# Kernel optimization log

Measured on AMD Instinct MI355X. Metric: run time of the kernel, lower is better.

## Reference

```python
import jax, jax.numpy as jnp
import numpy as np
from jax import lax

STATE = 16
DNA = 4


def _sobel_kernels():
    sx = jnp.array([[-1.0, 0.0, 1.0], [-2.0, 0.0, 2.0], [-1.0, 0.0, 1.0]], dtype=jnp.float32)
    sy = sx.T
    # depthwise kernels, OIHW with I=1, O=STATE
    kx = jnp.tile(sx[None, None], (STATE, 1, 1, 1))
    ky = jnp.tile(sy[None, None], (STATE, 1, 1, 1))
    return kx, ky


def _depthwise(x, k):
    # x: [B, C, H, W], k: [C, 1, 3, 3]; torch conv2d == cross-correlation == lax conv
    return lax.conv_general_dilated(
        x, k, window_strides=(1, 1), padding='SAME',
        feature_group_count=STATE,
        dimension_numbers=('NCHW', 'OIHW', 'NCHW'))


def setup_inputs() -> dict:
    key = jax.random.key(0)
    k1, k2, k3, k4 = jax.random.split(key, 4)
    B, H, W = 16, 256, 256
    x = jax.random.normal(k1, (B, STATE, H, W), dtype=jnp.float32)
    dna = jax.random.normal(k2, (B, DNA, H, W), dtype=jnp.float32)
    fan1 = STATE * 3 + DNA  # 52
    w1 = jax.random.normal(k3, (128, fan1), dtype=jnp.float32) * (1.0 / np.sqrt(fan1))
    w2 = jax.random.normal(k4, (STATE, 128), dtype=jnp.float32) * (1.0 / np.sqrt(128.0))
    return {"x": x, "dna": dna, "w1": w1, "w2": w2}


def reference(x, dna, w1, w2):
    kx, ky = _sobel_kernels()
    grad_x = _depthwise(x, kx)
    grad_y = _depthwise(x, ky)
    feat = jnp.concatenate([x, grad_x, grad_y, dna], axis=1)  # [B, 52, H, W]
    h = jnp.einsum('oc,bchw->bohw', w1, feat)  # 1x1 conv, bias=False
    h = jax.nn.relu(h)
    update = jnp.einsum('oc,bchw->bohw', w2, h)  # 1x1 conv to state_size
    return update
```

## Files before the change

### kernel.cpp

```cpp
#include <hip/hip_runtime.h>
#include <hip/hip_bf16.h>

#define STATE 16
#define DNA_C 4
#define HID   128
#define FAN1  52
#define HH    256
#define WW    256
#define HW    (HH * WW)

typedef unsigned short u16;
typedef unsigned int   u32;
typedef short bf8 __attribute__((ext_vector_type(8)));
typedef float f32x4 __attribute__((ext_vector_type(4)));

typedef __attribute__((address_space(1))) const void gv_t;
typedef __attribute__((address_space(3))) void lv_t;

__device__ __forceinline__ u32 pk(float a, float b) {
    __hip_bfloat162 t = __float22bfloat162_rn(make_float2(a, b));
    union { __hip_bfloat162 h; u32 u; } c; c.h = t; return c.u;
}
__device__ __forceinline__ u16 f2bf(float f) {
    union { __hip_bfloat16 h; u16 u; } c; c.h = __float2bfloat16(f); return c.u;
}

__global__ void prep_weights(const float* __restrict__ w1, const float* __restrict__ w2,
                             u16* __restrict__ wb) {
    int i = blockIdx.x * 256 + threadIdx.x;
    if (i < 128 * 64) {
        int p = i >> 6, knew = i & 63;
        int m = p >> 4, g = (p >> 2) & 3, r = p & 3;
        int hrow = 32 * (m >> 1) + 8 * g + 4 * (m & 1) + r;
        int w = knew >> 4, t = knew & 15;
        float v = 0.f;
        if (t < 4)        v = w1[hrow * FAN1 + 4 * w + t];
        else if (t < 8)   v = w1[hrow * FAN1 + 16 + 4 * w + (t - 4)];
        else if (t < 12)  v = w1[hrow * FAN1 + 32 + 4 * w + (t - 8)];
        else if (t == 12) v = w1[hrow * FAN1 + 48 + w];
        wb[i] = f2bf(v);
    } else if (i < 128 * 64 + 16 * 128) {
        wb[i] = f2bf(w2[i - 128 * 64]);
    }
}

__global__ __launch_bounds__(256, 2) void update_net24(
    const float* __restrict__ x,
    const float* __restrict__ dna,
    const u16*   __restrict__ wb,
    float* __restrict__ out,
    int nrows)
{
    __shared__ __align__(16) float raw_lds[3][STATE * WW];
    __shared__ __align__(16) u16 feat_lds[256 * 64];

    const int tid  = threadIdx.x;
    const int lane = tid & 63;
    const int wv   = tid >> 6;
    const int fj   = lane & 15;
    const int fg   = lane >> 4;
    const int f4   = fj >> 2;
    const int px0  = lane * 4;

    const u16* w1b = wb;
    const u16* w2b = wb + 128 * 64;
    bf8 a1[8][2];
    #pragma unroll
    for (int m = 0; m < 8; ++m) {
        #pragma unroll
        for (int kt = 0; kt < 2; ++kt)
            a1[m][kt] = *(const bf8*)&w1b[(16 * m + fj) * 64 + 32 * kt + 8 * fg];
    }
    bf8 a2[4];
    #pragma unroll
    for (int kt = 0; kt < 4; ++kt)
        a2[kt] = *(const bf8*)&w2b[fj * 128 + 32 * kt + 8 * fg];

    const f32x4 z0 = {0.f, 0.f, 0.f, 0.f};

    const int q  = nrows / gridDim.x;
    const int start = blockIdx.x * q;
    const int b  = start >> 8;
    const int y0 = start & 255;

    auto stage_row = [&](int yy, int slot) {
        const float* g = x + (((size_t)(b * STATE + 4 * wv)) * HH + yy) * WW + px0;
        float* l = &raw_lds[slot][(4 * wv) * WW];
        #pragma unroll
        for (int c = 0; c < 4; ++c)
            __builtin_amdgcn_global_load_lds((gv_t*)(g + (size_t)c * HW),
                                             (lv_t*)(l + c * WW), 16, 0, 0);
    };

    if (y0 > 0) stage_row(y0 - 1, (y0 - 1) % 3);
    stage_row(y0, y0 % 3);
    stage_row(y0 + 1, (y0 + 1) % 3);
    asm volatile("s_waitcnt vmcnt(0)" ::: "memory");
    __builtin_amdgcn_sched_barrier(0);

    for (int it = 0; it < q; ++it) {
        const int y = y0 + it;
        const bool ht = (y > 0), hb = (y < HH - 1);
        const int sm = y % 3, st3 = (y + 2) % 3, sb = (y + 1) % 3;

        {
            const f32x4 dnv = *(const f32x4*)(dna + (((size_t)(b * DNA_C + wv)) * HH + y) * WW + px0);
            const float* rm_ = &raw_lds[sm][(4 * wv) * WW + px0];
            const float* rt_ = &raw_lds[st3][(4 * wv) * WW + px0];
            const float* rb_ = &raw_lds[sb][(4 * wv) * WW + px0];

            f32x4 xm[4], gx[4], gy[4];
            #pragma unroll
            for (int c = 0; c < 4; ++c) {
                f32x4 m4 = *(const f32x4*)(rm_ + c * WW);
                f32x4 t4 = {0.f,0.f,0.f,0.f}, b4 = {0.f,0.f,0.f,0.f};
                if (ht) t4 = *(const f32x4*)(rt_ + c * WW);
                if (hb) b4 = *(const f32x4*)(rb_ + c * WW);
                f32x4 cs, d;
                #pragma unroll
                for (int i = 0; i < 4; ++i) {
                    cs[i] = fmaf(2.f, m4[i], t4[i] + b4[i]);
                    d[i]  = b4[i] - t4[i];
                }
                float csL = __shfl_up(cs[3], 1);
                float csR = __shfl_down(cs[0], 1);
                float dL  = __shfl_up(d[3], 1);
                float dR  = __shfl_down(d[0], 1);
                if (lane == 0)  { csL = 0.f; dL = 0.f; }
                if (lane == 63) { csR = 0.f; dR = 0.f; }
                xm[c] = m4;
                gx[c][0] = cs[1] - csL;   gx[c][1] = cs[2] - cs[0];
                gx[c][2] = cs[3] - cs[1]; gx[c][3] = csR - cs[2];
                gy[c][0] = fmaf(2.f, d[0], dL + d[1]);
                gy[c][1] = fmaf(2.f, d[1], d[0] + d[2]);
                gy[c][2] = fmaf(2.f, d[2], d[1] + d[3]);
                gy[c][3] = fmaf(2.f, d[3], d[2] + dR);
            }

            const int s = lane & 7;
            #pragma unroll
            for (int i = 0; i < 4; ++i) {
                u16* rowp = &feat_lds[(px0 + i) * 64];
                uint4 c0 = make_uint4(pk(xm[0][i], xm[1][i]), pk(xm[2][i], xm[3][i]),
                                      pk(gx[0][i], gx[1][i]), pk(gx[2][i], gx[3][i]));
                uint4 c1 = make_uint4(pk(gy[0][i], gy[1][i]), pk(gy[2][i], gy[3][i]),
                                      pk(dnv[i], 0.f), 0u);
                *(uint4*)&rowp[8 * ((2 * wv)     ^ s)] = c0;
                *(uint4*)&rowp[8 * ((2 * wv + 1) ^ s)] = c1;
            }
        }

        __syncthreads();

        if (it + 1 < q && y + 2 <= HH - 1)
            stage_row(y + 2, (y + 2) % 3);

        #pragma unroll
        for (int g4 = 0; g4 < 4; ++g4) {
            const int r  = wv * 64 + g4 * 16 + fj;
            const int sg = (4 * g4 + f4) & 7;
            bf8 b0 = *(const bf8*)&feat_lds[r * 64 + 8 * ((0 + fg) ^ sg)];
            bf8 b1 = *(const bf8*)&feat_lds[r * 64 + 8 * ((4 + fg) ^ sg)];

            u32 w[8][2];
            #pragma unroll
            for (int mh = 0; mh < 2; ++mh) {
                f32x4 hc[4];
                #pragma unroll
                for (int mm = 0; mm < 4; ++mm) {
                    const int m = mh * 4 + mm;
                    f32x4 z = __builtin_amdgcn_mfma_f32_16x16x32_bf16(a1[m][0], b0, z0, 0, 0, 0);
                    hc[mm] = __builtin_amdgcn_mfma_f32_16x16x32_bf16(a1[m][1], b1, z, 0, 0, 0);
                }
                #pragma unroll
                for (int mm = 0; mm < 4; ++mm) {
                    const int m = mh * 4 + mm;
                    w[m][0] = pk(fmaxf(hc[mm][0], 0.f), fmaxf(hc[mm][1], 0.f));
                    w[m][1] = pk(fmaxf(hc[mm][2], 0.f), fmaxf(hc[mm][3], 0.f));
                }
            }

            f32x4 uacc;
            #pragma unroll
            for (int kt = 0; kt < 4; ++kt) {
                union { u32 u[4]; bf8 v; } bb;
                bb.u[0] = w[2 * kt][0];
                bb.u[1] = w[2 * kt][1];
                bb.u[2] = w[2 * kt + 1][0];
                bb.u[3] = w[2 * kt + 1][1];
                uacc = __builtin_amdgcn_mfma_f32_16x16x32_bf16(a2[kt], bb.v,
                                                               (kt == 0) ? z0 : uacc, 0, 0, 0);
            }

            const int xo = wv * 64 + g4 * 16 + fj;
            float* po = out + (((size_t)(b * STATE + 4 * fg)) * HH + y) * WW + xo;
            #pragma unroll
            for (int rr2 = 0; rr2 < 4; ++rr2)
                po[(size_t)rr2 * HW] = uacc[rr2];
        }

        __syncthreads();
    }
}

extern "C" void kernel_launch(void* const* d_in, const int* in_sizes, int n_in,
                              void* d_out, int out_size, void* d_ws, size_t ws_size,
                              hipStream_t stream) {
    const float* x   = (const float*)d_in[0];
    const float* dna = (const float*)d_in[1];
    const float* w1  = (const float*)d_in[2];
    const float* w2  = (const float*)d_in[3];
    float* out = (float*)d_out;
    u16* wb = (u16*)d_ws;

    prep_weights<<<dim3(40), dim3(256), 0, stream>>>(w1, w2, wb);

    const int B = in_sizes[0] / (STATE * HH * WW);
    const int nrows = B * HH;
    const int grid = 512;
    update_net24<<<dim3(grid), dim3(256), 0, stream>>>(x, dna, wb, out, nrows);
}
```

Baseline: 52.85 us.

## Double block size to 8 waves, each handling 2 channels and 32 pixels

```diff
diff --git a/kernel.cpp b/kernel.cpp
--- a/kernel.cpp
+++ b/kernel.cpp
@@ -32,19 +32,19 @@
         int p = i >> 6, knew = i & 63;
         int m = p >> 4, g = (p >> 2) & 3, r = p & 3;
         int hrow = 32 * (m >> 1) + 8 * g + 4 * (m & 1) + r;
-        int w = knew >> 4, t = knew & 15;
+        int w = knew >> 3, s = knew & 7;
         float v = 0.f;
-        if (t < 4)        v = w1[hrow * FAN1 + 4 * w + t];
-        else if (t < 8)   v = w1[hrow * FAN1 + 16 + 4 * w + (t - 4)];
-        else if (t < 12)  v = w1[hrow * FAN1 + 32 + 4 * w + (t - 8)];
-        else if (t == 12) v = w1[hrow * FAN1 + 48 + w];
+        if (s < 2)                 v = w1[hrow * FAN1 + 2 * w + s];
+        else if (s < 4)            v = w1[hrow * FAN1 + 16 + 2 * w + (s - 2)];
+        else if (s < 6)            v = w1[hrow * FAN1 + 32 + 2 * w + (s - 4)];
+        else if (s == 6 && w < 4)  v = w1[hrow * FAN1 + 48 + w];
         wb[i] = f2bf(v);
     } else if (i < 128 * 64 + 16 * 128) {
         wb[i] = f2bf(w2[i - 128 * 64]);
     }
 }
 
-__global__ __launch_bounds__(256, 2) void update_net24(
+__global__ __launch_bounds__(512, 2) void update_net26(
     const float* __restrict__ x,
     const float* __restrict__ dna,
     const u16*   __restrict__ wb,
@@ -59,8 +59,8 @@
     const int wv   = tid >> 6;
     const int fj   = lane & 15;
     const int fg   = lane >> 4;
-    const int f4   = fj >> 2;
     const int px0  = lane * 4;
+    const int sw   = lane & 7;
 
     const u16* w1b = wb;
     const u16* w2b = wb + 128 * 64;
@@ -84,10 +84,10 @@
     const int y0 = start & 255;
 
     auto stage_row = [&](int yy, int slot) {
-        const float* g = x + (((size_t)(b * STATE + 4 * wv)) * HH + yy) * WW + px0;
-        float* l = &raw_lds[slot][(4 * wv) * WW];
+        const float* g = x + (((size_t)(b * STATE + 2 * wv)) * HH + yy) * WW + px0;
+        float* l = &raw_lds[slot][(2 * wv) * WW];
         #pragma unroll
-        for (int c = 0; c < 4; ++c)
+        for (int c = 0; c < 2; ++c)
             __builtin_amdgcn_global_load_lds((gv_t*)(g + (size_t)c * HW),
                                              (lv_t*)(l + c * WW), 16, 0, 0);
     };
@@ -97,6 +97,7 @@
     stage_row(y0 + 1, (y0 + 1) % 3);
     asm volatile("s_waitcnt vmcnt(0)" ::: "memory");
     __builtin_amdgcn_sched_barrier(0);
+    __syncthreads();
 
     for (int it = 0; it < q; ++it) {
         const int y = y0 + it;
@@ -104,14 +105,16 @@
         const int sm = y % 3, st3 = (y + 2) % 3, sb = (y + 1) % 3;
 
         {
-            const f32x4 dnv = *(const f32x4*)(dna + (((size_t)(b * DNA_C + wv)) * HH + y) * WW + px0);
-            const float* rm_ = &raw_lds[sm][(4 * wv) * WW + px0];
-            const float* rt_ = &raw_lds[st3][(4 * wv) * WW + px0];
-            const float* rb_ = &raw_lds[sb][(4 * wv) * WW + px0];
-
-            f32x4 xm[4], gx[4], gy[4];
-            #pragma unroll
-            for (int c = 0; c < 4; ++c) {
+            f32x4 dnv = {0.f, 0.f, 0.f, 0.f};
+            if (wv < DNA_C)
+                dnv = *(const f32x4*)(dna + (((size_t)(b * DNA_C + wv)) * HH + y) * WW + px0);
+            const float* rm_ = &raw_lds[sm][(2 * wv) * WW + px0];
+            const float* rt_ = &raw_lds[st3][(2 * wv) * WW + px0];
+            const float* rb_ = &raw_lds[sb][(2 * wv) * WW + px0];
+
+            f32x4 xm[2], gx[2], gy[2];
+            #pragma unroll
+            for (int c = 0; c < 2; ++c) {
                 f32x4 m4 = *(const f32x4*)(rm_ + c * WW);
                 f32x4 t4 = {0.f,0.f,0.f,0.f}, b4 = {0.f,0.f,0.f,0.f};
                 if (ht) t4 = *(const f32x4*)(rt_ + c * WW);
@@ -137,16 +140,13 @@
                 gy[c][3] = fmaf(2.f, d[3], d[2] + dR);
             }
 
-            const int s = lane & 7;
             #pragma unroll
             for (int i = 0; i < 4; ++i) {
-                u16* rowp = &feat_lds[(px0 + i) * 64];
-                uint4 c0 = make_uint4(pk(xm[0][i], xm[1][i]), pk(xm[2][i], xm[3][i]),
-                                      pk(gx[0][i], gx[1][i]), pk(gx[2][i], gx[3][i]));
-                uint4 c1 = make_uint4(pk(gy[0][i], gy[1][i]), pk(gy[2][i], gy[3][i]),
-                                      pk(dnv[i], 0.f), 0u);
-                *(uint4*)&rowp[8 * ((2 * wv)     ^ s)] = c0;
-                *(uint4*)&rowp[8 * ((2 * wv + 1) ^ s)] = c1;
+                uint4 qv = make_uint4(pk(xm[0][i], xm[1][i]),
+                                      pk(gx[0][i], gx[1][i]),
+                                      pk(gy[0][i], gy[1][i]),
+                                      pk(dnv[i], 0.f));
+                *(uint4*)&feat_lds[(px0 + i) * 64 + 8 * (wv ^ sw)] = qv;
             }
         }
 
@@ -154,15 +154,16 @@
 
         if (it + 1 < q && y + 2 <= HH - 1)
             stage_row(y + 2, (y + 2) % 3);
+        __builtin_amdgcn_sched_barrier(0);
 
         #pragma unroll
-        for (int g4 = 0; g4 < 4; ++g4) {
-            const int r  = wv * 64 + g4 * 16 + fj;
-            const int sg = (4 * g4 + f4) & 7;
-            bf8 b0 = *(const bf8*)&feat_lds[r * 64 + 8 * ((0 + fg) ^ sg)];
+        for (int g2 = 0; g2 < 2; ++g2) {
+            const int r  = 32 * wv + g2 * 16 + fj;
+            const int sg = (r >> 2) & 7;
+            bf8 b0 = *(const bf8*)&feat_lds[r * 64 + 8 * (fg ^ sg)];
             bf8 b1 = *(const bf8*)&feat_lds[r * 64 + 8 * ((4 + fg) ^ sg)];
 
-            u32 w[8][2];
+            f32x4 uacc;
             #pragma unroll
             for (int mh = 0; mh < 2; ++mh) {
                 f32x4 hc[4];
@@ -172,31 +173,29 @@
                     f32x4 z = __builtin_amdgcn_mfma_f32_16x16x32_bf16(a1[m][0], b0, z0, 0, 0, 0);
                     hc[mm] = __builtin_amdgcn_mfma_f32_16x16x32_bf16(a1[m][1], b1, z, 0, 0, 0);
                 }
+                u32 w[4][2];
                 #pragma unroll
                 for (int mm = 0; mm < 4; ++mm) {
-                    const int m = mh * 4 + mm;
-                    w[m][0] = pk(fmaxf(hc[mm][0], 0.f), fmaxf(hc[mm][1], 0.f));
-                    w[m][1] = pk(fmaxf(hc[mm][2], 0.f), fmaxf(hc[mm][3], 0.f));
+                    w[mm][0] = pk(fmaxf(hc[mm][0], 0.f), fmaxf(hc[mm][1], 0.f));
+                    w[mm][1] = pk(fmaxf(hc[mm][2], 0.f), fmaxf(hc[mm][3], 0.f));
+                }
+                #pragma unroll
+                for (int j = 0; j < 2; ++j) {
+                    union { u32 u[4]; bf8 v; } bb;
+                    bb.u[0] = w[2 * j][0];
+                    bb.u[1] = w[2 * j][1];
+                    bb.u[2] = w[2 * j + 1][0];
+                    bb.u[3] = w[2 * j + 1][1];
+                    uacc = __builtin_amdgcn_mfma_f32_16x16x32_bf16(
+                        a2[2 * mh + j], bb.v, (mh == 0 && j == 0) ? z0 : uacc, 0, 0, 0);
                 }
             }
 
-            f32x4 uacc;
-            #pragma unroll
-            for (int kt = 0; kt < 4; ++kt) {
-                union { u32 u[4]; bf8 v; } bb;
-                bb.u[0] = w[2 * kt][0];
-                bb.u[1] = w[2 * kt][1];
-                bb.u[2] = w[2 * kt + 1][0];
-                bb.u[3] = w[2 * kt + 1][1];
-                uacc = __builtin_amdgcn_mfma_f32_16x16x32_bf16(a2[kt], bb.v,
-                                                               (kt == 0) ? z0 : uacc, 0, 0, 0);
-            }
-
-            const int xo = wv * 64 + g4 * 16 + fj;
+            const int xo = 32 * wv + g2 * 16 + fj;
             float* po = out + (((size_t)(b * STATE + 4 * fg)) * HH + y) * WW + xo;
             #pragma unroll
-            for (int rr2 = 0; rr2 < 4; ++rr2)
-                po[(size_t)rr2 * HW] = uacc[rr2];
+            for (int rr = 0; rr < 4; ++rr)
+                po[(size_t)rr * HW] = uacc[rr];
         }
 
         __syncthreads();
@@ -218,5 +217,5 @@
     const int B = in_sizes[0] / (STATE * HH * WW);
     const int nrows = B * HH;
     const int grid = 512;
-    update_net24<<<dim3(grid), dim3(256), 0, stream>>>(x, dna, wb, out, nrows);
-}
+    update_net26<<<dim3(grid), dim3(512), 0, stream>>>(x, dna, wb, out, nrows);
+}
```

New measurement: 60.90 us. 15.2% more time.

## Software-pipeline Sobel features and MLP over half-row stages with double-buffered LDS

Applied to the files above, without the earlier changes.

```diff
diff --git a/kernel.cpp b/kernel.cpp
--- a/kernel.cpp
+++ b/kernel.cpp
@@ -13,6 +13,7 @@
 typedef unsigned int   u32;
 typedef short bf8 __attribute__((ext_vector_type(8)));
 typedef float f32x4 __attribute__((ext_vector_type(4)));
+typedef float f32x2 __attribute__((ext_vector_type(2)));
 
 typedef __attribute__((address_space(1))) const void gv_t;
 typedef __attribute__((address_space(3))) void lv_t;
@@ -44,7 +45,7 @@
     }
 }
 
-__global__ __launch_bounds__(256, 2) void update_net24(
+__global__ __launch_bounds__(256, 2) void update_net28(
     const float* __restrict__ x,
     const float* __restrict__ dna,
     const u16*   __restrict__ wb,
@@ -52,15 +53,15 @@
     int nrows)
 {
     __shared__ __align__(16) float raw_lds[3][STATE * WW];
-    __shared__ __align__(16) u16 feat_lds[256 * 64];
+    __shared__ __align__(16) u16 featA[128 * 64];
+    __shared__ __align__(16) u16 featB[128 * 64];
 
     const int tid  = threadIdx.x;
     const int lane = tid & 63;
     const int wv   = tid >> 6;
     const int fj   = lane & 15;
     const int fg   = lane >> 4;
-    const int f4   = fj >> 2;
-    const int px0  = lane * 4;
+    const int px0g = lane * 4;
 
     const u16* w1b = wb;
     const u16* w2b = wb + 128 * 64;
@@ -84,7 +85,7 @@
     const int y0 = start & 255;
 
     auto stage_row = [&](int yy, int slot) {
-        const float* g = x + (((size_t)(b * STATE + 4 * wv)) * HH + yy) * WW + px0;
+        const float* g = x + (((size_t)(b * STATE + 4 * wv)) * HH + yy) * WW + px0g;
         float* l = &raw_lds[slot][(4 * wv) * WW];
         #pragma unroll
         for (int c = 0; c < 4; ++c)
@@ -92,75 +93,69 @@
                                              (lv_t*)(l + c * WW), 16, 0, 0);
     };
 
-    if (y0 > 0) stage_row(y0 - 1, (y0 - 1) % 3);
-    stage_row(y0, y0 % 3);
-    stage_row(y0 + 1, (y0 + 1) % 3);
-    asm volatile("s_waitcnt vmcnt(0)" ::: "memory");
-    __builtin_amdgcn_sched_barrier(0);
-
-    for (int it = 0; it < q; ++it) {
-        const int y = y0 + it;
+    auto feature_half = [&](int y, int h, u16* fbuf) {
         const bool ht = (y > 0), hb = (y < HH - 1);
-        const int sm = y % 3, st3 = (y + 2) % 3, sb = (y + 1) % 3;
-
-        {
-            const f32x4 dnv = *(const f32x4*)(dna + (((size_t)(b * DNA_C + wv)) * HH + y) * WW + px0);
-            const float* rm_ = &raw_lds[sm][(4 * wv) * WW + px0];
-            const float* rt_ = &raw_lds[st3][(4 * wv) * WW + px0];
-            const float* rb_ = &raw_lds[sb][(4 * wv) * WW + px0];
-
-            f32x4 xm[4], gx[4], gy[4];
-            #pragma unroll
-            for (int c = 0; c < 4; ++c) {
-                f32x4 m4 = *(const f32x4*)(rm_ + c * WW);
-                f32x4 t4 = {0.f,0.f,0.f,0.f}, b4 = {0.f,0.f,0.f,0.f};
-                if (ht) t4 = *(const f32x4*)(rt_ + c * WW);
-                if (hb) b4 = *(const f32x4*)(rb_ + c * WW);
-                f32x4 cs, d;
-                #pragma unroll
-                for (int i = 0; i < 4; ++i) {
-                    cs[i] = fmaf(2.f, m4[i], t4[i] + b4[i]);
-                    d[i]  = b4[i] - t4[i];
-                }
-                float csL = __shfl_up(cs[3], 1);
-                float csR = __shfl_down(cs[0], 1);
-                float dL  = __shfl_up(d[3], 1);
-                float dR  = __shfl_down(d[0], 1);
-                if (lane == 0)  { csL = 0.f; dL = 0.f; }
-                if (lane == 63) { csR = 0.f; dR = 0.f; }
-                xm[c] = m4;
-                gx[c][0] = cs[1] - csL;   gx[c][1] = cs[2] - cs[0];
-                gx[c][2] = cs[3] - cs[1]; gx[c][3] = csR - cs[2];
-                gy[c][0] = fmaf(2.f, d[0], dL + d[1]);
-                gy[c][1] = fmaf(2.f, d[1], d[0] + d[2]);
-                gy[c][2] = fmaf(2.f, d[2], d[1] + d[3]);
-                gy[c][3] = fmaf(2.f, d[3], d[2] + dR);
+        const int sm = y % 3, st = (y + 2) % 3, sb = (y + 1) % 3;
+        const int px = 128 * h + 2 * lane;
+        const f32x2 dn2 = *(const f32x2*)(dna + (((size_t)(b * DNA_C + wv)) * HH + y) * WW + px);
+
+        float sx[4][2], gx[4][2], gy[4][2];
+        #pragma unroll
+        for (int c = 0; c < 4; ++c) {
+            const float* rm = &raw_lds[sm][(4 * wv + c) * WW];
+            const float* rt = &raw_lds[st][(4 * wv + c) * WW];
+            const float* rb = &raw_lds[sb][(4 * wv + c) * WW];
+            f32x2 m2 = *(const f32x2*)(rm + px);
+            f32x2 t2 = {0.f, 0.f}, b2 = {0.f, 0.f};
+            if (ht) t2 = *(const f32x2*)(rt + px);
+            if (hb) b2 = *(const f32x2*)(rb + px);
+            const float cs0 = fmaf(2.f, m2[0], t2[0] + b2[0]);
+            const float cs1 = fmaf(2.f, m2[1], t2[1] + b2[1]);
+            const float d0  = b2[0] - t2[0];
+            const float d1  = b2[1] - t2[1];
+            float csE = 0.f, dE = 0.f;
+            const bool lo = (lane == 0), hi = (lane == 63);
+            const bool useE = lo ? (h == 1) : (hi ? (h == 0) : false);
+            if (useE) {
+                const int ec = lo ? 127 : 128;
+                const float mE = rm[ec];
+                const float tE = ht ? rt[ec] : 0.f;
+                const float bE = hb ? rb[ec] : 0.f;
+                csE = fmaf(2.f, mE, tE + bE);
+                dE  = bE - tE;
             }
-
-            const int s = lane & 7;
-            #pragma unroll
-            for (int i = 0; i < 4; ++i) {
-                u16* rowp = &feat_lds[(px0 + i) * 64];
-                uint4 c0 = make_uint4(pk(xm[0][i], xm[1][i]), pk(xm[2][i], xm[3][i]),
-                                      pk(gx[0][i], gx[1][i]), pk(gx[2][i], gx[3][i]));
-                uint4 c1 = make_uint4(pk(gy[0][i], gy[1][i]), pk(gy[2][i], gy[3][i]),
-                                      pk(dnv[i], 0.f), 0u);
-                *(uint4*)&rowp[8 * ((2 * wv)     ^ s)] = c0;
-                *(uint4*)&rowp[8 * ((2 * wv + 1) ^ s)] = c1;
-            }
-        }
-
-        __syncthreads();
-
-        if (it + 1 < q && y + 2 <= HH - 1)
-            stage_row(y + 2, (y + 2) % 3);
-
-        #pragma unroll
-        for (int g4 = 0; g4 < 4; ++g4) {
-            const int r  = wv * 64 + g4 * 16 + fj;
-            const int sg = (4 * g4 + f4) & 7;
-            bf8 b0 = *(const bf8*)&feat_lds[r * 64 + 8 * ((0 + fg) ^ sg)];
-            bf8 b1 = *(const bf8*)&feat_lds[r * 64 + 8 * ((4 + fg) ^ sg)];
+            float csL = __shfl_up(cs1, 1);
+            float csR = __shfl_down(cs0, 1);
+            float dL  = __shfl_up(d1, 1);
+            float dR  = __shfl_down(d0, 1);
+            if (lo) { csL = csE; dL = dE; }
+            if (hi) { csR = csE; dR = dE; }
+            sx[c][0] = m2[0];          sx[c][1] = m2[1];
+            gx[c][0] = cs1 - csL;      gx[c][1] = csR - cs0;
+            gy[c][0] = fmaf(2.f, d0, dL + d1);
+            gy[c][1] = fmaf(2.f, d1, d0 + dR);
+        }
+        const int sW = (lane >> 1) & 7;
+        #pragma unroll
+        for (int i = 0; i < 2; ++i) {
+            const int lpx = 2 * lane + i;
+            u16* rowp = &fbuf[lpx * 64];
+            uint4 c0 = make_uint4(pk(sx[0][i], sx[1][i]), pk(sx[2][i], sx[3][i]),
+                                  pk(gx[0][i], gx[1][i]), pk(gx[2][i], gx[3][i]));
+            uint4 c1 = make_uint4(pk(gy[0][i], gy[1][i]), pk(gy[2][i], gy[3][i]),
+                                  pk(dn2[i], 0.f), 0u);
+            *(uint4*)&rowp[8 * ((2 * wv)     ^ sW)] = c0;
+            *(uint4*)&rowp[8 * ((2 * wv + 1) ^ sW)] = c1;
+        }
+    };
+
+    auto mlp_half = [&](int y, int h, const u16* fbuf) {
+        #pragma unroll
+        for (int g2 = 0; g2 < 2; ++g2) {
+            const int r  = 32 * wv + 16 * g2 + fj;
+            const int sg = (r >> 2) & 7;
+            bf8 b0 = *(const bf8*)&fbuf[r * 64 + 8 * ((0 + fg) ^ sg)];
+            bf8 b1 = *(const bf8*)&fbuf[r * 64 + 8 * ((4 + fg) ^ sg)];
 
             u32 w[8][2];
             #pragma unroll
@@ -179,7 +174,6 @@
                     w[m][1] = pk(fmaxf(hc[mm][2], 0.f), fmaxf(hc[mm][3], 0.f));
                 }
             }
-
             f32x4 uacc;
             #pragma unroll
             for (int kt = 0; kt < 4; ++kt) {
@@ -191,16 +185,46 @@
                 uacc = __builtin_amdgcn_mfma_f32_16x16x32_bf16(a2[kt], bb.v,
                                                                (kt == 0) ? z0 : uacc, 0, 0, 0);
             }
-
-            const int xo = wv * 64 + g4 * 16 + fj;
+            const int xo = 128 * h + 32 * wv + 16 * g2 + fj;
             float* po = out + (((size_t)(b * STATE + 4 * fg)) * HH + y) * WW + xo;
             #pragma unroll
-            for (int rr2 = 0; rr2 < 4; ++rr2)
-                po[(size_t)rr2 * HW] = uacc[rr2];
-        }
+            for (int rr = 0; rr < 4; ++rr)
+                po[(size_t)rr * HW] = uacc[rr];
+        }
+    };
+
+    if (y0 > 0) stage_row(y0 - 1, (y0 - 1) % 3);
+    stage_row(y0, y0 % 3);
+    stage_row(y0 + 1, (y0 + 1) % 3);
+    asm volatile("s_waitcnt vmcnt(0)" ::: "memory");
+    __builtin_amdgcn_sched_barrier(0);
+    __syncthreads();
+
+    const int S = 2 * q;
+    for (int s = 0; s < S; ++s) {
+        const int y = y0 + (s >> 1);
+        const int h = s & 1;
+        const bool do_stage = (h == 0) && (s > 0) && (y + 1 <= HH - 1);
+        if (do_stage)
+            stage_row(y + 1, (y + 1) % 3);
+
+        if (s > 0) {
+            const int yp = y0 + ((s - 1) >> 1);
+            const int hp = (s - 1) & 1;
+            mlp_half(yp, hp, hp ? featB : featA);
+        }
+
+        if (do_stage) {
+            __builtin_amdgcn_sched_barrier(0);
+            asm volatile("s_waitcnt vmcnt(8)" ::: "memory");
+            __builtin_amdgcn_sched_barrier(0);
+        }
+
+        feature_half(y, h, h ? featB : featA);
 
         __syncthreads();
     }
+    mlp_half(y0 + q - 1, 1, featB);
 }
 
 extern "C" void kernel_launch(void* const* d_in, const int* in_sizes, int n_in,
@@ -218,5 +242,5 @@
     const int B = in_sizes[0] / (STATE * HH * WW);
     const int nrows = B * HH;
     const int grid = 512;
-    update_net24<<<dim3(grid), dim3(256), 0, stream>>>(x, dna, wb, out, nrows);
-}
+    update_net28<<<dim3(grid), dim3(256), 0, stream>>>(x, dna, wb, out, nrows);
+}
```

Result: slower. 62.26 us (+17.8%).
